# Performance work log

Hardware: AMD Instinct MI355X
Metric: run time of the kernel (lower is better)

## Reference

```python
import jax, jax.numpy as jnp
import numpy as np

EMB_DIM = 256
DICT_SIZE = 8192
EPSILON = 1e-05


def setup_inputs() -> dict:
    key = jax.random.key(0)
    k_x, k_e = jax.random.split(key)
    x = jax.random.normal(k_x, (32, EMB_DIM, 32, 32), dtype=jnp.float32)
    embed = jax.random.normal(k_e, (DICT_SIZE, EMB_DIM), dtype=jnp.float32)
    embed = embed / jnp.linalg.norm(embed, axis=1, keepdims=True)  # F.normalize p=2
    track_num = jnp.zeros((DICT_SIZE, 1), dtype=jnp.float32)
    track_enc = embed  # buffers initialized as embed.clone()
    return {"x": x, "embed": embed, "track_num": track_num, "track_enc": track_enc}


def reference(x, embed, track_num, track_enc):
    b, c, h, w = x.shape
    K = embed.shape[0]
    # flatten: transpose(1,-1) -> [b,w,h,c], reshape -> [N, c]
    flat = jnp.transpose(x, (0, 3, 2, 1)).reshape(-1, c)  # [N, D]

    # KNN (k=1, l2): squared distance is monotone in l2, argmin identical
    x2 = jnp.sum(flat * flat, axis=1, keepdims=True)          # [N,1]
    e2 = jnp.sum(embed * embed, axis=1)                        # [K]
    d2 = x2 - 2.0 * (flat @ embed.T) + e2[None, :]             # [N,K]
    ids = jnp.argmin(d2, axis=1)                               # [N] int

    vqs_flat = embed[ids]                                      # [N, D]

    # EMA update, first-time path: buffers copied from raw statistics
    counts = jax.ops.segment_sum(jnp.ones_like(flat[:, 0]), ids, num_segments=K)
    new_track_num = counts[:, None]                            # [K,1]
    new_track_enc = jax.ops.segment_sum(flat, ids, num_segments=K)  # onehot.T @ flatten
    factor = 1.0 + EPSILON * K / new_track_num.sum()
    new_embed = new_track_enc * factor / (new_track_num + EPSILON)

    # restore spatial layout: view(b,w,h,c).transpose(1,-1) -> [b,c,h,w]
    vqs = jnp.transpose(vqs_flat.reshape(b, w, h, c), (0, 3, 2, 1))
    ids_out = jnp.transpose(ids.reshape(b, w, h), (0, 2, 1))   # [b,h,w]

    st_out = x + jax.lax.stop_gradient(vqs - x)                # straight-through
    loss = jnp.mean((jax.lax.stop_gradient(vqs) - x) ** 2)     # mse(vqs.detach(), input)
    return st_out, loss, ids_out, new_embed, new_track_num, new_track_enc
```

## Files before the change

kernel.cpp:

```cpp
#include <hip/hip_runtime.h>

#define NR 32768
#define CD 256
#define KD 8192

typedef __attribute__((ext_vector_type(8))) _Float16 f16x8;
typedef __attribute__((ext_vector_type(4))) _Float16 f16x4;
typedef __attribute__((ext_vector_type(4))) float f32x4;

#define F_XH      0ull
#define F_XL      4194304ull
#define F_EH      8388608ull
#define F_EMBT    9437184ull
#define F_E2N     11534336ull
#define F_E2NP    11542528ull
#define F_IDS     11550720ull
#define F_FLAGCNT 11583488ull
#define F_LOSS    11583489ull
#define F_FLAGLST 11583490ull
#define F_COUNTS  11616258ull
#define F_CURSOR  11624450ull
#define F_OFFS    11632642ull
#define F_BUCKET  11640834ull
#define F_PBD     11673602ull
#define F_PBI     11689986ull

#define OUT_ST   0ull
#define OUT_LOSS 8388608ull
#define OUT_IDS  8388609ull
#define OUT_NEMB 8421377ull
#define OUT_NUM  10518529ull
#define OUT_ENC  10526721ull

__device__ __forceinline__ float np_pw128(const float* p) {
    float r0 = p[0], r1 = p[1], r2 = p[2], r3 = p[3];
    float r4 = p[4], r5 = p[5], r6 = p[6], r7 = p[7];
    for (int i = 8; i < 128; i += 8) {
        r0 += p[i + 0]; r1 += p[i + 1]; r2 += p[i + 2]; r3 += p[i + 3];
        r4 += p[i + 4]; r5 += p[i + 5]; r6 += p[i + 6]; r7 += p[i + 7];
    }
    return ((r0 + r1) + (r2 + r3)) + ((r4 + r5) + (r6 + r7));
}

__global__ void k_cvt_x(const float* __restrict__ x,
                        _Float16* __restrict__ xh, _Float16* __restrict__ xl) {
    __shared__ float t[32 * 529];
    const int bx = blockIdx.x;
    const int b = bx >> 4, cg = (bx >> 1) & 7, h0 = (bx & 1) * 16;
    const int tid = threadIdx.x;
    const float* src = x + ((size_t)(b * 256 + cg * 32)) * 1024 + h0 * 32;
    for (int i = 0; i < 64; ++i) {
        int e = i * 256 + tid;
        int c = e >> 9, rem = e & 511;
        int hh = rem >> 5, w = rem & 31;
        t[c * 529 + hh * 33 + w] = src[(size_t)c * 1024 + hh * 32 + w];
    }
    __syncthreads();
    const int nj = tid >> 3;
    const int c4 = (tid & 7) * 4;
    #pragma unroll 4
    for (int i = 0; i < 16; ++i) {
        const int ns = i * 32 + nj;
        const int w = ns >> 4, hh = ns & 15;
        f16x4 hv, lv;
        #pragma unroll
        for (int j = 0; j < 4; ++j) {
            const float v = t[(c4 + j) * 529 + hh * 33 + w];
            const _Float16 hi = (_Float16)v;
            hv[j] = hi;
            lv[j] = (_Float16)(v - (float)hi);
        }
        const size_t o = ((size_t)(b * 1024 + w * 32 + h0 + hh)) * 256 + cg * 32 + c4;
        *(f16x4*)&xh[o] = hv;
        *(f16x4*)&xl[o] = lv;
    }
}

__global__ void k_prep_e(const float* __restrict__ embed,
                         _Float16* __restrict__ eh, float* __restrict__ e2n) {
    int wave = threadIdx.x >> 6, lane = threadIdx.x & 63;
    int k = blockIdx.x * 4 + wave;
    float4 v = *(const float4*)(embed + (size_t)k * CD + lane * 4);
    f16x4 h;
    h[0] = (_Float16)v.x; h[1] = (_Float16)v.y;
    h[2] = (_Float16)v.z; h[3] = (_Float16)v.w;
    *(f16x4*)&eh[(size_t)k * CD + lane * 4] = h;
    float s = v.x * v.x + v.y * v.y + v.z * v.z + v.w * v.w;
    #pragma unroll
    for (int off = 1; off < 64; off <<= 1) s += __shfl_xor(s, off);
    if (lane == 0) e2n[k] = -0.5f * s;
}

__global__ void k_e2np(const float* __restrict__ embed, float* __restrict__ e2np) {
    const int lane = threadIdx.x & 63;
    const int wv = threadIdx.x >> 6;
    const int k = blockIdx.x * 32 + wv * 8 + (lane >> 3);
    const int j = lane & 7;
    float hsum[2];
    #pragma unroll
    for (int half = 0; half < 2; ++half) {
        float r = 0.f;
        for (int i = 0; i < 16; ++i) {
            float v = embed[(size_t)k * CD + half * 128 + j + i * 8];
            float sq = v * v;
            asm volatile("" : "+v"(sq));
            r += sq;
        }
        float s = r + __shfl_xor(r, 1);
        s = s + __shfl_xor(s, 2);
        s = s + __shfl_xor(s, 4);
        hsum[half] = s;
    }
    if (j == 0) e2np[k] = hsum[0] + hsum[1];
}

__global__ void k_epose(const float* __restrict__ embed, float* __restrict__ embedT) {
    int kt = blockIdx.x >> 2, ct = blockIdx.x & 3;
    __shared__ float t[64][65];
    int tid = threadIdx.x;
    #pragma unroll
    for (int i = 0; i < 16; ++i) {
        int e = tid + i * 256; int r = e >> 6, c = e & 63;
        t[r][c] = embed[(size_t)(kt * 64 + r) * CD + ct * 64 + c];
    }
    __syncthreads();
    #pragma unroll
    for (int i = 0; i < 16; ++i) {
        int e = tid + i * 256; int c = e >> 6, r = e & 63;
        embedT[(size_t)(ct * 64 + c) * KD + kt * 64 + r] = t[r][c];
    }
}

#define LDSB 0
#define LDSA 65536
#define LDSM 131072
__global__ __launch_bounds__(512, 1) void k_mfma(
    const _Float16* __restrict__ xh, const _Float16* __restrict__ eh,
    const float* __restrict__ e2n, int* __restrict__ ids,
    int* __restrict__ flag_cnt, int* __restrict__ flag_list,
    int* __restrict__ counts)
{
    __shared__ char smem[131072 + 6144];
    const int tid = threadIdx.x;
    const int w = tid >> 6, l = tid & 63;
    const int wm = w & 3, wn = w >> 2;
    const int lr = l & 15, q = l >> 4;
    const int n0 = blockIdx.x * 128;

    #pragma unroll
    for (int i = 0; i < 8; ++i) {
        const int row = i * 16 + (tid >> 5);
        const int slot = tid & 31;
        const _Float16* src = xh + (size_t)(n0 + row) * 256 + ((slot ^ (row & 15)) * 8);
        __builtin_amdgcn_global_load_lds(
            (const __attribute__((address_space(1))) unsigned int*)src,
            (__attribute__((address_space(3))) unsigned int*)(smem + LDSB + row * 512 + slot * 16),
            16, 0, 0);
    }

    auto STAGE_A = [&](int s, int bufc) {
        if (s < 256) {
            const int bufo = LDSA + bufc * 16384;
            #pragma unroll
            for (int i = 0; i < 2; ++i) {
                const int code = i * 128 + (tid >> 2);
                const int slot = tid & 3;
                const _Float16* src = eh + (size_t)((s >> 3) * 256 + code) * 256
                                         + (s & 7) * 32 + ((slot ^ ((code >> 1) & 3)) * 8);
                __builtin_amdgcn_global_load_lds(
                    (const __attribute__((address_space(1))) unsigned int*)src,
                    (__attribute__((address_space(3))) unsigned int*)
                        (smem + bufo + code * 64 + slot * 16),
                    16, 0, 0);
            }
        } else {
            #pragma unroll
            for (int i = 0; i < 2; ++i) {
                __builtin_amdgcn_global_load_lds(
                    (const __attribute__((address_space(1))) unsigned int*)(eh + tid * 8),
                    (__attribute__((address_space(3))) unsigned int*)
                        (smem + LDSM + i * 1024 + (tid & 63) * 16),
                    16, 0, 0);
            }
        }
    };

    f32x4 e2c[4];
    #pragma unroll
    for (int m = 0; m < 4; ++m)
        e2c[m] = *(const f32x4*)(e2n + wm * 64 + m * 16 + q * 4);
    STAGE_A(0, 0); STAGE_A(1, 1); STAGE_A(2, 2);
    __builtin_amdgcn_sched_barrier(0);
    asm volatile("s_waitcnt vmcnt(4)" ::: "memory");
    __builtin_amdgcn_s_barrier();
    __builtin_amdgcn_sched_barrier(0);

    f32x4 acc[4][4];
    float m1[4], m2[4]; int i1[4];
    #pragma unroll
    for (int n = 0; n < 4; ++n) { m1[n] = -3.4e38f; m2[n] = -3.4e38f; i1[n] = 0; }

    int faoff[4];
    #pragma unroll
    for (int m = 0; m < 4; ++m) {
        const int code = wm * 64 + m * 16 + lr;
        faoff[m] = LDSA + code * 64 + ((q ^ ((code >> 1) & 3)) * 16);
    }
    int fboff[4], rx[4];
    #pragma unroll
    for (int n = 0; n < 4; ++n) {
        const int row = wn * 64 + n * 16 + lr;
        fboff[n] = LDSB + row * 512;
        rx[n] = row & 15;
    }

    #pragma unroll 1
    for (int cg = 0; cg < 32; ++cg) {
        #pragma unroll
        for (int cc = 0; cc < 8; ++cc) {
            const int s = cg * 8 + cc;
            if (cc == 6 && cg < 31) {
                #pragma unroll
                for (int m = 0; m < 4; ++m)
                    e2c[m] = *(const f32x4*)(e2n + (cg + 1) * 256 + wm * 64 + m * 16 + q * 4);
            }
            STAGE_A(s + 3, (cc + 3) & 3);
            const int bufo = LDSA + (cc & 3) * 16384;
            f16x8 fa[4], fb[4];
            #pragma unroll
            for (int m = 0; m < 4; ++m)
                fa[m] = *(const f16x8*)(smem + bufo + faoff[m] - LDSA);
            #pragma unroll
            for (int n = 0; n < 4; ++n) {
                const int g = cc * 4 + q;
                fb[n] = *(const f16x8*)(smem + fboff[n] + ((g ^ rx[n]) * 16));
            }
            if (cc == 0) {
                #pragma unroll
                for (int m = 0; m < 4; ++m)
                    #pragma unroll
                    for (int n = 0; n < 4; ++n)
                        acc[m][n] = __builtin_amdgcn_mfma_f32_16x16x32_f16(fa[m], fb[n], e2c[m], 0, 0, 0);
            } else {
                #pragma unroll
                for (int m = 0; m < 4; ++m)
                    #pragma unroll
                    for (int n = 0; n < 4; ++n)
                        acc[m][n] = __builtin_amdgcn_mfma_f32_16x16x32_f16(fa[m], fb[n], acc[m][n], 0, 0, 0);
            }
            if (cc == 7) {
                const int kb = cg * 256 + wm * 64 + q * 4;
                #pragma unroll
                for (int n = 0; n < 4; ++n)
                    #pragma unroll
                    for (int m = 0; m < 4; ++m)
                        #pragma unroll
                        for (int r = 0; r < 4; ++r) {
                            const float v = acc[m][n][r];
                            const bool g = v > m1[n];
                            m2[n] = fmaxf(m2[n], fminf(v, m1[n]));
                            m1[n] = fmaxf(m1[n], v);
                            i1[n] = g ? (kb + m * 16 + r) : i1[n];
                        }
            }
            __builtin_amdgcn_sched_barrier(0);
            asm volatile("s_waitcnt vmcnt(4)" ::: "memory");
            __builtin_amdgcn_s_barrier();
            __builtin_amdgcn_sched_barrier(0);
        }
    }

    #pragma unroll
    for (int off = 16; off < 64; off <<= 1) {
        #pragma unroll
        for (int n = 0; n < 4; ++n) {
            const float om1 = __shfl_xor(m1[n], off);
            const float om2 = __shfl_xor(m2[n], off);
            const int   oi  = __shfl_xor(i1[n], off);
            const bool g = om1 > m1[n];
            m2[n] = fmaxf(fminf(m1[n], om1), fmaxf(m2[n], om2));
            m1[n] = fmaxf(m1[n], om1);
            i1[n] = g ? oi : i1[n];
        }
    }
    float* sm1 = (float*)(smem + LDSM);
    float* sm2 = (float*)(smem + LDSM + 2048);
    int*   si1 = (int*)  (smem + LDSM + 4096);
    __syncthreads();
    if (q == 0) {
        #pragma unroll
        for (int n = 0; n < 4; ++n) {
            const int row = wn * 64 + n * 16 + lr;
            sm1[wm * 128 + row] = m1[n];
            sm2[wm * 128 + row] = m2[n];
            si1[wm * 128 + row] = i1[n];
        }
    }
    __syncthreads();
    if (tid < 128) {
        float a1 = sm1[tid], a2 = sm2[tid]; int ai = si1[tid];
        #pragma unroll
        for (int wq = 1; wq < 4; ++wq) {
            const float b1 = sm1[wq * 128 + tid], b2 = sm2[wq * 128 + tid];
            const int bi = si1[wq * 128 + tid];
            const bool g = b1 > a1;
            a2 = fmaxf(fminf(a1, b1), fmaxf(a2, b2));
            a1 = fmaxf(a1, b1);
            ai = g ? bi : ai;
        }
        const int n = n0 + tid;
        ids[n] = ai;
        atomicAdd(&counts[ai], 1);
        if (a1 - a2 < 2.5e-3f) {
            int p = atomicAdd(flag_cnt, 1);
            flag_list[p] = n;
        }
    }
}

#define RG 16
__global__ __launch_bounds__(256) void k_rescore(
    const float* __restrict__ x, const float* __restrict__ embedT,
    const float* __restrict__ e2np, const int* __restrict__ flag_cnt,
    const int* __restrict__ flag_list, float* __restrict__ pbd, int* __restrict__ pbi)
{
    __shared__ float rowl[RG][256];
    __shared__ float sq[RG][256];
    __shared__ float x2s[RG];
    __shared__ float bdA[256];
    __shared__ int   biA[256];
    const int tid = threadIdx.x;
    int cnt = *flag_cnt; if (cnt > 2048) cnt = 2048;
    const int ngroups = (cnt + RG - 1) / RG;
    const int kt = blockIdx.x & 7;
    for (int g = blockIdx.x >> 3; g < ngroups; g += 64) {
        #pragma unroll
        for (int i = 0; i < RG; ++i) {
            int f = g * RG + i;
            float v = 0.f;
            if (f < cnt) {
                int n = flag_list[f];
                int b = n >> 10, wq = (n >> 5) & 31, hq = n & 31;
                v = x[((size_t)(b * 256 + tid)) * 1024 + hq * 32 + wq];
            }
            rowl[i][tid] = v;
            sq[i][tid] = v * v;
        }
        __syncthreads();
        if (tid < RG) x2s[tid] = np_pw128(sq[tid]) + np_pw128(sq[tid] + 128);
        __syncthreads();

        float acc[RG][4];
        #pragma unroll
        for (int r = 0; r < RG; ++r)
            #pragma unroll
            for (int e = 0; e < 4; ++e) acc[r][e] = 0.f;
        for (int c = 0; c < 256; ++c) {
            const f32x4 bv = *(const f32x4*)&embedT[(size_t)c * KD + kt * 1024 + tid * 4];
            #pragma unroll
            for (int r = 0; r < RG; ++r) {
                const float av = rowl[r][c];
                acc[r][0] = fmaf(av, bv[0], acc[r][0]);
                acc[r][1] = fmaf(av, bv[1], acc[r][1]);
                acc[r][2] = fmaf(av, bv[2], acc[r][2]);
                acc[r][3] = fmaf(av, bv[3], acc[r][3]);
            }
        }
        #pragma unroll
        for (int r = 0; r < RG; ++r) {
            float bd = 3.4e38f; int bi = 0x7fffffff;
            #pragma unroll
            for (int e = 0; e < 4; ++e) {
                const int k = kt * 1024 + tid * 4 + e;
                const float d2 = (x2s[r] - 2.0f * acc[r][e]) + e2np[k];
                if (d2 < bd || (d2 == bd && k < bi)) { bd = d2; bi = k; }
            }
            bdA[tid] = bd; biA[tid] = bi;
            __syncthreads();
            for (int off = 128; off > 0; off >>= 1) {
                if (tid < off) {
                    float od = bdA[tid + off]; int oi = biA[tid + off];
                    if (od < bdA[tid] || (od == bdA[tid] && oi < biA[tid])) {
                        bdA[tid] = od; biA[tid] = oi;
                    }
                }
                __syncthreads();
            }
            if (tid == 0) {
                int f = g * RG + r;
                if (f < cnt) { pbd[f * 8 + kt] = bdA[0]; pbi[f * 8 + kt] = biA[0]; }
            }
            __syncthreads();
        }
    }
}

__global__ void k_flagmerge(const int* __restrict__ flag_cnt, const int* __restrict__ flag_list,
                            const float* __restrict__ pbd, const int* __restrict__ pbi,
                            int* __restrict__ ids, int* __restrict__ counts) {
    int cnt = *flag_cnt; if (cnt > 2048) cnt = 2048;
    int f = blockIdx.x * 256 + threadIdx.x;
    if (f >= cnt) return;
    float bd = pbd[f * 8]; int bi = pbi[f * 8];
    #pragma unroll
    for (int kt = 1; kt < 8; ++kt) {
        float d = pbd[f * 8 + kt]; int i = pbi[f * 8 + kt];
        if (d < bd || (d == bd && i < bi)) { bd = d; bi = i; }
    }
    const int n = flag_list[f];
    const int old = ids[n];
    if (bi != old) {
        ids[n] = bi;
        atomicAdd(&counts[old], -1);
        atomicAdd(&counts[bi], 1);
    }
}

__global__ __launch_bounds__(256) void k_output(
    const float* __restrict__ x, const float* __restrict__ embed,
    const int* __restrict__ ids, float* __restrict__ st,
    float* __restrict__ loss_ws)
{
    const int b = blockIdx.x >> 5, h = blockIdx.x & 31;
    const int tid = threadIdx.x;
    __shared__ int sid[32];
    __shared__ float vq[256 * 33];
    if (tid < 32) sid[tid] = ids[b * 1024 + tid * 32 + h];
    __syncthreads();
    #pragma unroll 4
    for (int w = 0; w < 32; ++w) {
        vq[tid * 33 + w] = embed[(size_t)sid[w] * CD + tid];
    }
    __syncthreads();
    float lsum = 0.f;
    const size_t base0 = (((size_t)b * 256) * 32 + h) * 32;
    #pragma unroll 8
    for (int it = 0; it < 32; ++it) {
        const int c = it * 8 + (tid >> 5);
        const int w = tid & 31;
        const size_t a = base0 + (size_t)c * 1024 + w;
        const float v = vq[c * 33 + w];
        const float xv = x[a];
        st[a] = v;
        const float d = v - xv;
        lsum = fmaf(d, d, lsum);
    }
    #pragma unroll
    for (int off = 1; off < 64; off <<= 1) lsum += __shfl_xor(lsum, off);
    if ((tid & 63) == 0) atomicAdd(loss_ws, lsum);
}

__global__ void k_scan(const int* __restrict__ counts, int* __restrict__ offs,
                       float* __restrict__ track_num) {
    __shared__ int ps[257];
    const int tid = threadIdx.x;
    int loc[32]; int s = 0;
    const int base = tid * 32;
    #pragma unroll
    for (int j = 0; j < 32; ++j) { loc[j] = s; s += counts[base + j]; }
    ps[tid + 1] = s;
    if (tid == 0) ps[0] = 0;
    __syncthreads();
    if (tid == 0) for (int i = 1; i <= 256; ++i) ps[i] += ps[i - 1];
    __syncthreads();
    const int pre = ps[tid];
    #pragma unroll
    for (int j = 0; j < 32; ++j) {
        offs[base + j] = pre + loc[j];
        track_num[base + j] = (float)counts[base + j];
    }
}

__global__ void k_fill(const int* __restrict__ ids, const int* __restrict__ offs,
                       int* __restrict__ cursor, int* __restrict__ bucket,
                       float* __restrict__ ids_out) {
    int n = blockIdx.x * 256 + threadIdx.x;
    int id = ids[n];
    int p = atomicAdd(&cursor[id], 1);
    bucket[offs[id] + p] = n;
    int b = n >> 10, w = (n >> 5) & 31, h = n & 31;
    ids_out[b * 1024 + h * 32 + w] = (float)id;
}

__global__ void k_gather(const _Float16* __restrict__ xh, const _Float16* __restrict__ xl,
                         const int* __restrict__ offs, const int* __restrict__ counts,
                         const int* __restrict__ bucket, float* __restrict__ enc) {
    const int k = blockIdx.x, c = threadIdx.x;
    const int o = offs[k], cnt = counts[k];
    float s = 0.f;
    for (int i = 0; i < cnt; ++i) {
        int n = bucket[o + i];
        s += (float)xh[(size_t)n * CD + c] + (float)xl[(size_t)n * CD + c];
    }
    enc[(size_t)k * CD + c] = s;
}

__global__ void k_final(const float* __restrict__ track_num, const float* __restrict__ track_enc,
                        float* __restrict__ new_embed, const float* __restrict__ loss_ws,
                        float* __restrict__ loss_out)
{
    const size_t e = (size_t)blockIdx.x * 256 + threadIdx.x;
    const int k = (int)(e >> 8);
    const float factor = 1.0f + (1e-5f * 8192.0f) / 32768.0f;
    new_embed[e] = track_enc[e] * factor / (track_num[k] + 1e-5f);
    if (e == 0) loss_out[0] = loss_ws[0] * (1.0f / 8388608.0f);
}

extern "C" void kernel_launch(void* const* d_in, const int* in_sizes, int n_in,
                              void* d_out, int out_size, void* d_ws, size_t ws_size,
                              hipStream_t stream)
{
    const float* x     = (const float*)d_in[0];
    const float* embed = (const float*)d_in[1];
    float* out = (float*)d_out;
    float* ws  = (float*)d_ws;

    _Float16* xh = (_Float16*)(ws + F_XH);
    _Float16* xl = (_Float16*)(ws + F_XL);
    _Float16* eh = (_Float16*)(ws + F_EH);
    float* embedT    = ws + F_EMBT;
    float* e2n       = ws + F_E2N;
    float* e2np      = ws + F_E2NP;
    int*   ids       = (int*)(ws + F_IDS);
    int*   flag_cnt  = (int*)(ws + F_FLAGCNT);
    float* loss_ws   = ws + F_LOSS;
    int*   flag_list = (int*)(ws + F_FLAGLST);
    int*   counts    = (int*)(ws + F_COUNTS);
    int*   cursor    = (int*)(ws + F_CURSOR);
    int*   offs      = (int*)(ws + F_OFFS);
    int*   bucket    = (int*)(ws + F_BUCKET);
    float* pbd       = ws + F_PBD;
    int*   pbi       = (int*)(ws + F_PBI);

    hipMemsetAsync(ws + F_FLAGCNT, 0, 2 * sizeof(float), stream);
    hipMemsetAsync(ws + F_COUNTS, 0, 2 * 8192 * sizeof(float), stream);

    k_cvt_x    <<<512,  256, 0, stream>>>(x, xh, xl);
    k_prep_e   <<<2048, 256, 0, stream>>>(embed, eh, e2n);
    k_e2np     <<<256,  256, 0, stream>>>(embed, e2np);
    k_epose    <<<512,  256, 0, stream>>>(embed, embedT);
    k_mfma     <<<256,  512, 0, stream>>>(xh, eh, e2n, ids, flag_cnt, flag_list, counts);
    k_rescore  <<<512,  256, 0, stream>>>(x, embedT, e2np, flag_cnt, flag_list, pbd, pbi);
    k_flagmerge<<<8,    256, 0, stream>>>(flag_cnt, flag_list, pbd, pbi, ids, counts);
    k_output   <<<1024, 256, 0, stream>>>(x, embed, ids, out + OUT_ST, loss_ws);
    k_scan     <<<1,    256, 0, stream>>>(counts, offs, out + OUT_NUM);
    k_fill     <<<128,  256, 0, stream>>>(ids, offs, cursor, bucket, out + OUT_IDS);
    k_gather   <<<8192, 256, 0, stream>>>(xh, xl, offs, counts, bucket, out + OUT_ENC);
    k_final    <<<8192, 256, 0, stream>>>(out + OUT_NUM, out + OUT_ENC, out + OUT_NEMB,
                                          loss_ws, out + OUT_LOSS);
}
```

Before: 370.7 us.

## Fuse embed prep kernels and final into gather; vectorize x transpose loads and output

Merges the two embedding preprocessing kernels into a single launch, and folds the new_embed/loss finalization into the gather kernel, computing it from the in-register sum and the count. It also switches the input-transpose load in the x conversion kernel and the straight-through output/loss loop to float4 accesses. Together these remove two kernel launches and a full re-read of track_enc, and they widen global memory transactions. The cost is more work per block in the fused kernels and a small change in floating-point accumulation order for the loss.

```diff
diff --git a/kernel.cpp b/kernel.cpp
--- a/kernel.cpp
+++ b/kernel.cpp
@@ -49,11 +49,14 @@
     const int b = bx >> 4, cg = (bx >> 1) & 7, h0 = (bx & 1) * 16;
     const int tid = threadIdx.x;
     const float* src = x + ((size_t)(b * 256 + cg * 32)) * 1024 + h0 * 32;
-    for (int i = 0; i < 64; ++i) {
-        int e = i * 256 + tid;
-        int c = e >> 9, rem = e & 511;
-        int hh = rem >> 5, w = rem & 31;
-        t[c * 529 + hh * 33 + w] = src[(size_t)c * 1024 + hh * 32 + w];
+    #pragma unroll 4
+    for (int i = 0; i < 16; ++i) {
+        const int e4 = i * 256 + tid;
+        const int c = e4 >> 7, rem = e4 & 127;
+        const int hh = rem >> 3, w4 = (rem & 7) * 4;
+        const float4 v = *(const float4*)(src + (size_t)c * 1024 + hh * 32 + w4);
+        float* dst = &t[c * 529 + hh * 33 + w4];
+        dst[0] = v.x; dst[1] = v.y; dst[2] = v.z; dst[3] = v.w;
     }
     __syncthreads();
     const int nj = tid >> 3;
@@ -76,24 +79,23 @@
     }
 }
 
-__global__ void k_prep_e(const float* __restrict__ embed,
-                         _Float16* __restrict__ eh, float* __restrict__ e2n) {
-    int wave = threadIdx.x >> 6, lane = threadIdx.x & 63;
-    int k = blockIdx.x * 4 + wave;
-    float4 v = *(const float4*)(embed + (size_t)k * CD + lane * 4);
-    f16x4 h;
-    h[0] = (_Float16)v.x; h[1] = (_Float16)v.y;
-    h[2] = (_Float16)v.z; h[3] = (_Float16)v.w;
-    *(f16x4*)&eh[(size_t)k * CD + lane * 4] = h;
-    float s = v.x * v.x + v.y * v.y + v.z * v.z + v.w * v.w;
-    #pragma unroll
-    for (int off = 1; off < 64; off <<= 1) s += __shfl_xor(s, off);
-    if (lane == 0) e2n[k] = -0.5f * s;
-}
-
-__global__ void k_e2np(const float* __restrict__ embed, float* __restrict__ e2np) {
+__global__ void k_prep_e2(const float* __restrict__ embed, _Float16* __restrict__ eh,
+                          float* __restrict__ e2n, float* __restrict__ e2np) {
     const int lane = threadIdx.x & 63;
     const int wv = threadIdx.x >> 6;
+    #pragma unroll
+    for (int i = 0; i < 8; ++i) {
+        const int k = blockIdx.x * 32 + wv * 8 + i;
+        const float4 v = *(const float4*)(embed + (size_t)k * CD + lane * 4);
+        f16x4 h;
+        h[0] = (_Float16)v.x; h[1] = (_Float16)v.y;
+        h[2] = (_Float16)v.z; h[3] = (_Float16)v.w;
+        *(f16x4*)&eh[(size_t)k * CD + lane * 4] = h;
+        float s = v.x * v.x + v.y * v.y + v.z * v.z + v.w * v.w;
+        #pragma unroll
+        for (int off = 1; off < 64; off <<= 1) s += __shfl_xor(s, off);
+        if (lane == 0) e2n[k] = -0.5f * s;
+    }
     const int k = blockIdx.x * 32 + wv * 8 + (lane >> 3);
     const int j = lane & 7;
     float hsum[2];
@@ -433,17 +435,24 @@
     }
     __syncthreads();
     float lsum = 0.f;
+    const int j4 = (tid & 7) * 4;
+    const int c0 = tid >> 3;
     const size_t base0 = (((size_t)b * 256) * 32 + h) * 32;
-    #pragma unroll 8
-    for (int it = 0; it < 32; ++it) {
-        const int c = it * 8 + (tid >> 5);
-        const int w = tid & 31;
-        const size_t a = base0 + (size_t)c * 1024 + w;
-        const float v = vq[c * 33 + w];
-        const float xv = x[a];
-        st[a] = v;
-        const float d = v - xv;
-        lsum = fmaf(d, d, lsum);
+    #pragma unroll
+    for (int it = 0; it < 8; ++it) {
+        const int c = it * 32 + c0;
+        const size_t a = base0 + (size_t)c * 1024 + j4;
+        const float4 xv = *(const float4*)(x + a);
+        float4 vv;
+        vv.x = vq[c * 33 + j4 + 0];
+        vv.y = vq[c * 33 + j4 + 1];
+        vv.z = vq[c * 33 + j4 + 2];
+        vv.w = vq[c * 33 + j4 + 3];
+        *(float4*)(st + a) = vv;
+        const float d0 = vv.x - xv.x, d1 = vv.y - xv.y;
+        const float d2 = vv.z - xv.z, d3 = vv.w - xv.w;
+        lsum = fmaf(d0, d0, lsum); lsum = fmaf(d1, d1, lsum);
+        lsum = fmaf(d2, d2, lsum); lsum = fmaf(d3, d3, lsum);
     }
     #pragma unroll
     for (int off = 1; off < 64; off <<= 1) lsum += __shfl_xor(lsum, off);
@@ -484,7 +493,9 @@
 
 __global__ void k_gather(const _Float16* __restrict__ xh, const _Float16* __restrict__ xl,
                          const int* __restrict__ offs, const int* __restrict__ counts,
-                         const int* __restrict__ bucket, float* __restrict__ enc) {
+                         const int* __restrict__ bucket, float* __restrict__ enc,
+                         float* __restrict__ nemb, const float* __restrict__ loss_ws,
+                         float* __restrict__ loss_out) {
     const int k = blockIdx.x, c = threadIdx.x;
     const int o = offs[k], cnt = counts[k];
     float s = 0.f;
@@ -493,17 +504,9 @@
         s += (float)xh[(size_t)n * CD + c] + (float)xl[(size_t)n * CD + c];
     }
     enc[(size_t)k * CD + c] = s;
-}
-
-__global__ void k_final(const float* __restrict__ track_num, const float* __restrict__ track_enc,
-                        float* __restrict__ new_embed, const float* __restrict__ loss_ws,
-                        float* __restrict__ loss_out)
-{
-    const size_t e = (size_t)blockIdx.x * 256 + threadIdx.x;
-    const int k = (int)(e >> 8);
     const float factor = 1.0f + (1e-5f * 8192.0f) / 32768.0f;
-    new_embed[e] = track_enc[e] * factor / (track_num[k] + 1e-5f);
-    if (e == 0) loss_out[0] = loss_ws[0] * (1.0f / 8388608.0f);
+    nemb[(size_t)k * CD + c] = s * factor / ((float)cnt + 1e-5f);
+    if (k == 0 && c == 0) loss_out[0] = loss_ws[0] * (1.0f / 8388608.0f);
 }
 
 extern "C" void kernel_launch(void* const* d_in, const int* in_sizes, int n_in,
@@ -536,8 +539,7 @@
     hipMemsetAsync(ws + F_COUNTS, 0, 2 * 8192 * sizeof(float), stream);
 
     k_cvt_x    <<<512,  256, 0, stream>>>(x, xh, xl);
-    k_prep_e   <<<2048, 256, 0, stream>>>(embed, eh, e2n);
-    k_e2np     <<<256,  256, 0, stream>>>(embed, e2np);
+    k_prep_e2  <<<256,  256, 0, stream>>>(embed, eh, e2n, e2np);
     k_epose    <<<512,  256, 0, stream>>>(embed, embedT);
     k_mfma     <<<256,  512, 0, stream>>>(xh, eh, e2n, ids, flag_cnt, flag_list, counts);
     k_rescore  <<<512,  256, 0, stream>>>(x, embedT, e2np, flag_cnt, flag_list, pbd, pbi);
@@ -545,7 +547,6 @@
     k_output   <<<1024, 256, 0, stream>>>(x, embed, ids, out + OUT_ST, loss_ws);
     k_scan     <<<1,    256, 0, stream>>>(counts, offs, out + OUT_NUM);
     k_fill     <<<128,  256, 0, stream>>>(ids, offs, cursor, bucket, out + OUT_IDS);
-    k_gather   <<<8192, 256, 0, stream>>>(xh, xl, offs, counts, bucket, out + OUT_ENC);
-    k_final    <<<8192, 256, 0, stream>>>(out + OUT_NUM, out + OUT_ENC, out + OUT_NEMB,
-                                          loss_ws, out + OUT_LOSS);
-}
+    k_gather   <<<8192, 256, 0, stream>>>(xh, xl, offs, counts, bucket, out + OUT_ENC,
+                                          out + OUT_NEMB, loss_ws, out + OUT_LOSS);
+}
```

Measured after the change: 364.4 us. Within noise of the previous version (-1.7%).
